# Performance work log

Hardware: AMD Instinct MI355X
Metric: run time of the kernel (lower is better)

The kernel has to match this reference:

```python
import jax, jax.numpy as jnp
import numpy as np
import math

N, C, H = 2048, 256, 8
D = C // H
T, R, E = 8, 12, 32768
BUCKETS = 21
SEED = 128


def _layernorm(x, g, b, eps=1e-5):
    mu = jnp.mean(x, axis=-1, keepdims=True)
    var = jnp.var(x, axis=-1, keepdims=True)
    return (x - mu) * jax.lax.rsqrt(var + eps) * g + b


def _bucketize_dt(dt, num_buckets):
    eps = 1e-06
    signed_log = jnp.sign(dt) * jnp.log1p(jnp.abs(dt) + eps)
    min_v, max_v = -5.0, 5.0
    norm = (jnp.clip(signed_log, min_v, max_v) - min_v) / (max_v - min_v + 1e-09)
    idx = jnp.floor(norm * (num_buckets - 1)).astype(jnp.int32)
    return jnp.clip(idx, 0, num_buckets - 1)


def setup_inputs() -> dict:
    key = jax.random.key(0)
    ks = jax.random.split(key, 24)
    s = 0.02
    inp = {
        'X': jax.random.normal(ks[0], (N, C), jnp.float32),
        'token_type': jax.random.randint(ks[1], (N,), 0, T, jnp.int32),
        'edge_src': jax.random.randint(ks[2], (E,), 0, N, jnp.int32),
        'edge_dst': jax.random.randint(ks[3], (E,), 0, N, jnp.int32),
        'edge_rel': jax.random.randint(ks[4], (E,), 0, R, jnp.int32),
        'time_vec': jax.random.normal(ks[5], (N,), jnp.float32),
        'seed_count': SEED,
        'Wq': jax.random.normal(ks[6], (C, C), jnp.float32) * s,
        'bq': jnp.zeros((C,), jnp.float32),
        'Wk': jax.random.normal(ks[7], (C, C), jnp.float32) * s,
        'bk': jnp.zeros((C,), jnp.float32),
        'Wv': jax.random.normal(ks[8], (C, C), jnp.float32) * s,
        'bv': jnp.zeros((C,), jnp.float32),
        'Wo': jax.random.normal(ks[9], (C, C), jnp.float32) * s,
        'bo': jnp.zeros((C,), jnp.float32),
        'ln1_g': jnp.ones((C,), jnp.float32),
        'ln1_b': jnp.zeros((C,), jnp.float32),
        'ln2_g': jnp.ones((C,), jnp.float32),
        'ln2_b': jnp.zeros((C,), jnp.float32),
        'W1': jax.random.normal(ks[10], (C, 4 * C), jnp.float32) * s,
        'b1': jnp.zeros((4 * C,), jnp.float32),
        'W2': jax.random.normal(ks[11], (4 * C, C), jnp.float32) * s,
        'b2': jnp.zeros((C,), jnp.float32),
        'adj_rel_bias': jnp.zeros((R, H), jnp.float32),
        'typepair_bias': jnp.zeros((T, T, H), jnp.float32),
        'temp_bias': jax.random.normal(ks[12], (BUCKETS, H), jnp.float32) * s,
    }
    return inp


def reference(X, token_type, edge_src, edge_dst, edge_rel, time_vec, seed_count,
              Wq, bq, Wk, bk, Wv, bv, Wo, bo,
              ln1_g, ln1_b, ln2_g, ln2_b, W1, b1, W2, b2,
              adj_rel_bias, typepair_bias, temp_bias):
    n = X.shape[0]
    h = _layernorm(X, ln1_g, ln1_b)
    q = (h @ Wq + bq).reshape(n, H, D)
    k = (h @ Wk + bk).reshape(n, H, D)
    v = (h @ Wv + bv).reshape(n, H, D)
    scores = jnp.einsum('nhd,mhd->hnm', q, k) / math.sqrt(D)  # [H, N, N]

    # structural bias, factored as [N, N, H] then transposed
    bias = typepair_bias[token_type][:, token_type]            # [N, N, H]
    bias = bias.at[edge_src, edge_dst].add(adj_rel_bias[edge_rel])
    # seed-wise temporal bias on the first seed_count rows
    dt = time_vec[None, :] - time_vec[:seed_count, None]       # [S, N]
    tb = temp_bias[_bucketize_dt(dt, BUCKETS)]                 # [S, N, H]
    bias = bias.at[:seed_count].add(tb)

    attn = jax.nn.softmax(scores + bias.transpose(2, 0, 1), axis=-1)
    o = jnp.einsum('hnm,mhd->nhd', attn, v).reshape(n, C)
    x = X + (o @ Wo + bo)

    h2 = _layernorm(x, ln2_g, ln2_b)
    f = jax.nn.gelu(h2 @ W1 + b1, approximate=False) @ W2 + b2
    return x + f
```

## Files before the change

kernel.cpp:

```cpp
#include <hip/hip_runtime.h>
#include <hip/hip_bf16.h>
#include <math.h>

#define NTOK 2048
#define CDIM 256
#define HHEADS 8
#define DHEAD 32
#define NEDGE 32768
#define NTILE 16
#define SPLITS 8
#define TPS 2
#define EXTD 64
#define LE 72

typedef __attribute__((ext_vector_type(8))) short short8;
typedef __attribute__((ext_vector_type(4))) short short4v;
typedef __attribute__((ext_vector_type(4))) float f32x4;

static __device__ inline short f2bf(float f) {
    __hip_bfloat16 h = __float2bfloat16(f);
    return *reinterpret_cast<short*>(&h);
}
static __device__ inline float bf2f(short s) {
    unsigned int u = ((unsigned int)(unsigned short)s) << 16;
    return *reinterpret_cast<float*>(&u);
}

__global__ __launch_bounds__(256) void ln4_kernel(const float* __restrict__ X,
    const float* __restrict__ g, const float* __restrict__ b, short* __restrict__ out)
{
    int t = threadIdx.x;
    int wv = t >> 6, lane = t & 63;
    int row = blockIdx.x * 4 + wv;

    float4 x = *(const float4*)&X[(size_t)row * CDIM + lane * 4];
    float s = x.x + x.y + x.z + x.w;
    #pragma unroll
    for (int off = 1; off < 64; off <<= 1) s += __shfl_xor(s, off);
    float mu = s * (1.0f / CDIM);
    float4 d = { x.x - mu, x.y - mu, x.z - mu, x.w - mu };
    float s2 = d.x * d.x + d.y * d.y + d.z * d.z + d.w * d.w;
    #pragma unroll
    for (int off = 1; off < 64; off <<= 1) s2 += __shfl_xor(s2, off);
    float rsig = rsqrtf(s2 * (1.0f / CDIM) + 1e-5f);
    float4 gg = *(const float4*)&g[lane * 4];
    float4 bb = *(const float4*)&b[lane * 4];
    short o4[4];
    o4[0] = f2bf(d.x * rsig * gg.x + bb.x);
    o4[1] = f2bf(d.y * rsig * gg.y + bb.y);
    o4[2] = f2bf(d.z * rsig * gg.z + bb.z);
    o4[3] = f2bf(d.w * rsig * gg.w + bb.w);
    *(short4v*)&out[(size_t)row * CDIM + lane * 4] = *(short4v*)o4;
}

static __device__ inline void transpose_tile_f32(const float* __restrict__ in,
    short* __restrict__ out, int K, int N, int k0, int n0, int t)
{
    __shared__ float tile[64][65];
    int r0 = t >> 4, c0 = (t & 15) * 4;
    #pragma unroll
    for (int i = 0; i < 4; i++) {
        int r = r0 + i * 16;
        float4 v = *(const float4*)(in + (size_t)(k0 + r) * N + n0 + c0);
        tile[r][c0 + 0] = v.x; tile[r][c0 + 1] = v.y;
        tile[r][c0 + 2] = v.z; tile[r][c0 + 3] = v.w;
    }
    __syncthreads();
    #pragma unroll
    for (int i = 0; i < 4; i++) {
        int nr = r0 + i * 16;
        short o4[4];
        #pragma unroll
        for (int j = 0; j < 4; j++) o4[j] = f2bf(tile[c0 + j][nr]);
        *(short4v*)(out + (size_t)(n0 + nr) * K + k0 + c0) = *(short4v*)o4;
    }
}

__global__ __launch_bounds__(256) void prep_kernel(
    const float* __restrict__ Wq, const float* __restrict__ Wk,
    const float* __restrict__ Wv, const float* __restrict__ Wo,
    const float* __restrict__ W1, const float* __restrict__ W2,
    short* __restrict__ wt_qkv, short* __restrict__ wot,
    short* __restrict__ w1t, short* __restrict__ w2t,
    const int* __restrict__ token_type, const float* __restrict__ typepair_bias,
    short* __restrict__ qh, short* __restrict__ kh,
    int* __restrict__ cnt2)
{
    int b = blockIdx.x;
    int t = threadIdx.x;
    if (b < 192) {
        const float* src; short* dst; int K, N, bx, by;
        if (b < 64) {
            int m = b >> 4, r = b & 15;
            src = (m == 0) ? Wq : (m == 1) ? Wk : (m == 2) ? Wv : Wo;
            dst = (m == 0) ? wt_qkv : (m == 1) ? wt_qkv + 256 * 256
                : (m == 2) ? wt_qkv + 512 * 256 : wot;
            K = 256; N = 256; bx = r & 3; by = r >> 2;
        } else if (b < 128) {
            int r = b - 64; src = W1; dst = w1t; K = 256; N = 1024; bx = r & 15; by = r >> 4;
        } else {
            int r = b - 128; src = W2; dst = w2t; K = 1024; N = 256; bx = r & 3; by = r >> 2;
        }
        transpose_tile_f32(src, dst, K, N, by * 64, bx * 64, t);
    } else if (b < 256) {
        int idx = (b - 192) * 256 + t;
        int row = idx >> 3, h = idx & 7;
        int tt = token_type[row];
        short qe[32], ke[32];
        #pragma unroll
        for (int j = 0; j < 32; j++) {
            if (j < 8) {
                qe[j] = f2bf(typepair_bias[(tt * 8 + j) * 8 + h]);
                ke[j] = (j == tt) ? (short)0x3F80 : (short)0;
            } else { qe[j] = 0; ke[j] = 0; }
        }
        size_t base = ((size_t)h * NTOK + row) * EXTD + 32;
        #pragma unroll
        for (int k = 0; k < 4; k++) {
            *(short8*)&qh[base + k * 8] = *(short8*)&qe[k * 8];
            *(short8*)&kh[base + k * 8] = *(short8*)&ke[k * 8];
        }
    } else {
        cnt2[(b - 256) * 256 + t] = 0;
        cnt2[(b - 256) * 256 + t + 8192] = 0;
        cnt2[(b - 256) * 256 + t + 16384] = 0;
        cnt2[(b - 256) * 256 + t + 24576] = 0;
    }
}

template<int EPI>
__global__ __launch_bounds__(256) void gemm32_kernel(
    const short* __restrict__ A, const short* __restrict__ Bt,
    const float* __restrict__ bias, const float* __restrict__ resid,
    void* __restrict__ out_, int M, int N, int K)
{
    __shared__ short A_lds[32 * 40];
    __shared__ short B_lds[64 * 40];

    const int t = threadIdx.x;
    const int w = t >> 6, lane = t & 63, c = lane & 15, g = lane >> 4;
    const int row0 = blockIdx.y * 32, col0 = blockIdx.x * 64;
    const int srow = t >> 2, sk = (t & 3) * 8;

    f32x4 acc[2] = {};

    for (int k0 = 0; k0 < K; k0 += 32) {
        if (t < 128)
            *(short8*)&A_lds[srow * 40 + sk] = *(const short8*)&A[(size_t)(row0 + srow) * K + k0 + sk];
        *(short8*)&B_lds[srow * 40 + sk] = *(const short8*)&Bt[(size_t)(col0 + srow) * K + k0 + sk];
        __syncthreads();
        short8 af = *(const short8*)&A_lds[((w & 1) * 16 + c) * 40 + g * 8];
        #pragma unroll
        for (int nf = 0; nf < 2; nf++) {
            short8 bf = *(const short8*)&B_lds[((w >> 1) * 32 + nf * 16 + c) * 40 + g * 8];
            acc[nf] = __builtin_amdgcn_mfma_f32_16x16x32_bf16(af, bf, acc[nf], 0, 0, 0);
        }
        __syncthreads();
    }

    #pragma unroll
    for (int nf = 0; nf < 2; nf++) {
        #pragma unroll
        for (int reg = 0; reg < 4; reg++) {
            int row = row0 + (w & 1) * 16 + g * 4 + reg;
            int col = col0 + (w >> 1) * 32 + nf * 16 + c;
            float v = acc[nf][reg] + bias[col];
            if (EPI == 2) {
                ((float*)out_)[(size_t)row * N + col] = v + resid[(size_t)row * N + col];
            } else {
                v = 0.5f * v * (1.0f + erff(v * 0.70710678118654752f));
                ((short*)out_)[(size_t)row * N + col] = f2bf(v);
            }
        }
    }
}

__global__ __launch_bounds__(256) void gemm32_qkv_kernel(
    const short* __restrict__ A, const short* __restrict__ Bt,
    const float* __restrict__ bq, const float* __restrict__ bk, const float* __restrict__ bv,
    short* __restrict__ qh, short* __restrict__ kh, short* __restrict__ vt)
{
    const int K = CDIM;
    __shared__ short A_lds[32 * 40];
    __shared__ short B_lds[64 * 40];

    const int t = threadIdx.x;
    const int w = t >> 6, lane = t & 63, c = lane & 15, g = lane >> 4;
    const int row0 = blockIdx.y * 32, col0 = blockIdx.x * 64;
    const int srow = t >> 2, sk = (t & 3) * 8;

    f32x4 acc[2] = {};

    for (int k0 = 0; k0 < K; k0 += 32) {
        if (t < 128)
            *(short8*)&A_lds[srow * 40 + sk] = *(const short8*)&A[(size_t)(row0 + srow) * K + k0 + sk];
        *(short8*)&B_lds[srow * 40 + sk] = *(const short8*)&Bt[(size_t)(col0 + srow) * K + k0 + sk];
        __syncthreads();
        short8 af = *(const short8*)&A_lds[((w & 1) * 16 + c) * 40 + g * 8];
        #pragma unroll
        for (int nf = 0; nf < 2; nf++) {
            short8 bf = *(const short8*)&B_lds[((w >> 1) * 32 + nf * 16 + c) * 40 + g * 8];
            acc[nf] = __builtin_amdgcn_mfma_f32_16x16x32_bf16(af, bf, acc[nf], 0, 0, 0);
        }
        __syncthreads();
    }

    const int region = col0 >> 8;
    const int colr0 = col0 & 255;
    const float* bias = (region == 0) ? bq : (region == 1) ? bk : bv;
    #pragma unroll
    for (int nf = 0; nf < 2; nf++) {
        #pragma unroll
        for (int reg = 0; reg < 4; reg++) {
            int row = row0 + (w & 1) * 16 + g * 4 + reg;
            int col = colr0 + (w >> 1) * 32 + nf * 16 + c;
            float v = acc[nf][reg] + bias[col];
            if (region == 0) v *= 0.17677669529663687f;
            short bb = f2bf(v);
            size_t hidx = ((size_t)(col >> 5) * NTOK + row) * EXTD + (col & 31);
            if (region == 0)      qh[hidx] = bb;
            else if (region == 1) kh[hidx] = bb;
            else                  vt[(size_t)col * NTOK + row] = bb;
        }
    }
}

__global__ void edge_hist2_kernel(const int* __restrict__ src, const int* __restrict__ dst,
    int* __restrict__ cnt, int E)
{
    int e = blockIdx.x * blockDim.x + threadIdx.x;
    if (e < E) atomicAdd(&cnt[src[e] * NTILE + (dst[e] >> 7)], 1);
}

__global__ __launch_bounds__(256) void edge_scan2_kernel(const int* __restrict__ cnt,
    int* __restrict__ row_ptr, int* __restrict__ wcur)
{
    __shared__ int sums[256];
    int t = threadIdx.x;
    int base = t * 128;
    int s = 0;
    for (int i = 0; i < 128; i++) s += cnt[base + i];
    sums[t] = s;
    __syncthreads();
    for (int off = 1; off < 256; off <<= 1) {
        int v = (t >= off) ? sums[t - off] : 0;
        __syncthreads();
        sums[t] += v;
        __syncthreads();
    }
    int run = (t == 0) ? 0 : sums[t - 1];
    for (int i = 0; i < 128; i++) {
        row_ptr[base + i] = run;
        wcur[base + i] = run;
        run += cnt[base + i];
    }
    if (t == 255) row_ptr[NTOK * NTILE] = run;
}

__global__ void edge_scatter2_kernel(const int* __restrict__ src, const int* __restrict__ dst,
    const int* __restrict__ rel, int* __restrict__ wcur, int2* __restrict__ pairs, int E)
{
    int e = blockIdx.x * blockDim.x + threadIdx.x;
    if (e < E) {
        int d = dst[e];
        int pos = atomicAdd(&wcur[src[e] * NTILE + (d >> 7)], 1);
        pairs[pos] = make_int2(d, rel[e]);
    }
}

__global__ __launch_bounds__(256) void sgemm_kernel(
    const short* __restrict__ qh, const short* __restrict__ kh,
    short* __restrict__ S)
{
    __shared__ short A_lds[64 * LE];
    __shared__ short B_lds[64 * LE];
    const int t = threadIdx.x;
    const int w = t >> 6, lane = t & 63, c = lane & 15, g = lane >> 4;
    const int h = blockIdx.z;
    const int m0 = blockIdx.x * 64, n0 = blockIdx.y * 64;

    {
        int r = t >> 3, off = (t & 7) * 8;
        *(short8*)&A_lds[r * LE + off] =
            *(const short8*)&qh[((size_t)h * NTOK + n0 + r) * EXTD + off];
        *(short8*)&A_lds[(r + 32) * LE + off] =
            *(const short8*)&qh[((size_t)h * NTOK + n0 + 32 + r) * EXTD + off];
        *(short8*)&B_lds[r * LE + off] =
            *(const short8*)&kh[((size_t)h * NTOK + m0 + r) * EXTD + off];
        *(short8*)&B_lds[(r + 32) * LE + off] =
            *(const short8*)&kh[((size_t)h * NTOK + m0 + 32 + r) * EXTD + off];
    }
    __syncthreads();

    short8 alo = *(const short8*)&A_lds[(w * 16 + c) * LE + g * 8];
    short8 ahi = *(const short8*)&A_lds[(w * 16 + c) * LE + 32 + g * 8];
    f32x4 acc[4] = {};
    #pragma unroll
    for (int nf = 0; nf < 4; nf++) {
        short8 blo = *(const short8*)&B_lds[(nf * 16 + c) * LE + g * 8];
        short8 bhi = *(const short8*)&B_lds[(nf * 16 + c) * LE + 32 + g * 8];
        acc[nf] = __builtin_amdgcn_mfma_f32_16x16x32_bf16(alo, blo, acc[nf], 0, 0, 0);
        acc[nf] = __builtin_amdgcn_mfma_f32_16x16x32_bf16(ahi, bhi, acc[nf], 0, 0, 0);
    }

    #pragma unroll
    for (int nf = 0; nf < 4; nf++)
        #pragma unroll
        for (int reg = 0; reg < 4; reg++) {
            int row = n0 + w * 16 + g * 4 + reg;
            int col = m0 + nf * 16 + c;
            S[((size_t)h * NTOK + row) * NTOK + col] = f2bf(acc[nf][reg]);
        }
}

__global__ __launch_bounds__(256) void softmax_kernel(
    short* __restrict__ S,
    const float* __restrict__ time_vec, const int* __restrict__ seed_ptr,
    const float* __restrict__ adj_rel_bias, const float* __restrict__ temp_bias,
    const int* __restrict__ row_ptr2, const int2* __restrict__ pairs2)
{
    __shared__ float rowbuf[4][NTOK];

    int t = threadIdx.x, wv = t >> 6, lane = t & 63;
    int task = blockIdx.x * 4 + wv;
    int h = task >> 11, n = task & 2047;
    int seed = seed_ptr[0];
    bool temporal = (n < seed);
    float tn = time_vec[n];
    float* rb = rowbuf[wv];
    short* Srow = &S[((size_t)h * NTOK + n) * NTOK];

    #pragma unroll
    for (int i = 0; i < 4; i++) {
        int m0 = i * 512 + lane * 8;
        short8 sv = *(const short8*)&Srow[m0];
        float v[8];
        #pragma unroll
        for (int j = 0; j < 8; j++) v[j] = bf2f(sv[j]);
        if (temporal) {
            float4 ta = *(const float4*)&time_vec[m0];
            float4 tb = *(const float4*)&time_vec[m0 + 4];
            float tv8[8] = { ta.x, ta.y, ta.z, ta.w, tb.x, tb.y, tb.z, tb.w };
            #pragma unroll
            for (int j = 0; j < 8; j++) {
                float dt = tv8[j] - tn;
                float ab = fabsf(dt) + 1e-6f;
                float sg = (dt > 0.0f) ? 1.0f : ((dt < 0.0f) ? -1.0f : 0.0f);
                float sl = sg * log1pf(ab);
                sl = fminf(fmaxf(sl, -5.0f), 5.0f);
                float norm = (sl + 5.0f) * (1.0f / (10.0f + 1e-9f));
                int bidx = (int)floorf(norm * 20.0f);
                bidx = min(max(bidx, 0), 20);
                v[j] += temp_bias[bidx * 8 + h];
            }
        }
        float4 lo = { v[0], v[1], v[2], v[3] };
        float4 hi = { v[4], v[5], v[6], v[7] };
        *(float4*)&rb[m0] = lo;
        *(float4*)&rb[m0 + 4] = hi;
    }
    __syncthreads();

    {
        int e0 = row_ptr2[n * NTILE], e1 = row_ptr2[(n + 1) * NTILE];
        for (int e = e0 + lane; e < e1; e += 64) {
            int2 pr = pairs2[e];
            atomicAdd(&rb[pr.x], adj_rel_bias[pr.y * 8 + h]);
        }
    }
    __syncthreads();

    float vv[32];
    float mx = -INFINITY;
    #pragma unroll
    for (int i = 0; i < 4; i++) {
        float4 a = *(const float4*)&rb[i * 512 + lane * 8];
        float4 b = *(const float4*)&rb[i * 512 + lane * 8 + 4];
        vv[i * 8 + 0] = a.x; vv[i * 8 + 1] = a.y; vv[i * 8 + 2] = a.z; vv[i * 8 + 3] = a.w;
        vv[i * 8 + 4] = b.x; vv[i * 8 + 5] = b.y; vv[i * 8 + 6] = b.z; vv[i * 8 + 7] = b.w;
    }
    #pragma unroll
    for (int i = 0; i < 32; i++) mx = fmaxf(mx, vv[i]);
    #pragma unroll
    for (int off = 1; off < 64; off <<= 1) mx = fmaxf(mx, __shfl_xor(mx, off));
    float sum = 0.0f;
    #pragma unroll
    for (int i = 0; i < 32; i++) { vv[i] = __expf(vv[i] - mx); sum += vv[i]; }
    #pragma unroll
    for (int off = 1; off < 64; off <<= 1) sum += __shfl_xor(sum, off);
    float inv = 1.0f / sum;

    #pragma unroll
    for (int i = 0; i < 4; i++) {
        short p8[8];
        #pragma unroll
        for (int j = 0; j < 8; j++) p8[j] = f2bf(vv[i * 8 + j] * inv);
        *(short8*)&Srow[i * 512 + lane * 8] = *(short8*)p8;
    }
}

__global__ __launch_bounds__(256) void pv_kernel(
    const short* __restrict__ P, const short* __restrict__ vt,
    short* __restrict__ o)
{
    __shared__ short A_lds[32 * LE];
    __shared__ short B_lds[32 * LE];
    const int t = threadIdx.x;
    const int w = t >> 6, lane = t & 63, c = lane & 15, g = lane >> 4;
    const int h = blockIdx.y;
    const int n0 = blockIdx.x * 32;
    const int rowblk = (w & 1) * 16, colblk = (w >> 1) * 16;

    f32x4 acc = {0.0f, 0.0f, 0.0f, 0.0f};

    for (int k0 = 0; k0 < NTOK; k0 += 64) {
        int r = t >> 3, off = (t & 7) * 8;
        *(short8*)&A_lds[r * LE + off] =
            *(const short8*)&P[((size_t)h * NTOK + n0 + r) * NTOK + k0 + off];
        *(short8*)&B_lds[r * LE + off] =
            *(const short8*)&vt[(size_t)(h * 32 + r) * NTOK + k0 + off];
        __syncthreads();
        short8 alo = *(const short8*)&A_lds[(rowblk + c) * LE + g * 8];
        short8 ahi = *(const short8*)&A_lds[(rowblk + c) * LE + 32 + g * 8];
        short8 blo = *(const short8*)&B_lds[(colblk + c) * LE + g * 8];
        short8 bhi = *(const short8*)&B_lds[(colblk + c) * LE + 32 + g * 8];
        acc = __builtin_amdgcn_mfma_f32_16x16x32_bf16(alo, blo, acc, 0, 0, 0);
        acc = __builtin_amdgcn_mfma_f32_16x16x32_bf16(ahi, bhi, acc, 0, 0, 0);
        __syncthreads();
    }

    #pragma unroll
    for (int reg = 0; reg < 4; reg++) {
        int row = n0 + rowblk + g * 4 + reg;
        int col = h * 32 + colblk + c;
        o[(size_t)row * CDIM + col] = f2bf(acc[reg]);
    }
}

#define QBLK 32
#define KBLK 128

__global__ __launch_bounds__(256) void attn_mfma3_kernel(
    const short* __restrict__ qh, const short* __restrict__ kh,
    const short* __restrict__ vt,
    const float* __restrict__ time_vec, const int* __restrict__ seed_ptr,
    const float* __restrict__ adj_rel_bias, const float* __restrict__ temp_bias,
    const int* __restrict__ row_ptr2, const int2* __restrict__ pairs2,
    float* __restrict__ Op_part, float2* __restrict__ ml_part)
{
    __shared__ __align__(16) short Q_lds[QBLK * LE];
    __shared__ __align__(16) short K_lds[KBLK * LE];
    __shared__ __align__(16) short Vt_lds[DHEAD * 136];
    __shared__ __align__(16) unsigned int P32[QBLK * 68];
    __shared__ float tcol_s[KBLK];
    __shared__ float temp_h[21];
    __shared__ float adj_h[12];
    __shared__ float2 ml[2][QBLK];

    const int h  = blockIdx.y;
    const int n0 = blockIdx.x * QBLK;
    const int sblk = blockIdx.z;
    const int t  = threadIdx.x;
    const int wv = t >> 6, lane = t & 63, c = lane & 15, g = lane >> 4;
    const int rowblk  = (wv & 1) * 16;
    const int halfIdx = wv >> 1;
    const int colhalf = halfIdx * 64;
    const int seed = seed_ptr[0];
    const bool blockTemporal = (n0 < seed);
    const int gt0 = sblk * TPS;

    {
        int row = t >> 3, off = (t & 7) * 8;
        *(short8*)&Q_lds[row * LE + off] =
            *(const short8*)&qh[((size_t)h * NTOK + n0 + row) * EXTD + off];
    }
    if (t < 21)  temp_h[t] = temp_bias[t * HHEADS + h];
    if (t < 12)  adj_h[t] = adj_rel_bias[t * HHEADS + h];

    const int nrow = n0 + rowblk + c;
    const bool rowTemporal = (nrow < seed);
    const float tn = time_vec[nrow];

    int2 rp01 = *(const int2*)&row_ptr2[nrow * NTILE + gt0];
    int  rp2  = row_ptr2[nrow * NTILE + gt0 + 2];

    const int krow = t >> 3, koff = (t & 7) * 8;
    const int vrow = t >> 4, voff = (t & 15) * 8;
    short8 kr0, kr1, kr2, kr3, vr0, vr1;
    float tcr = 0.0f;

    auto LOADT = [&](int gt) {
        int m0 = gt * KBLK;
        const short* kp = &kh[((size_t)h * NTOK + m0 + krow) * EXTD + koff];
        kr0 = *(const short8*)kp;
        kr1 = *(const short8*)(kp + (size_t)32 * EXTD);
        kr2 = *(const short8*)(kp + (size_t)64 * EXTD);
        kr3 = *(const short8*)(kp + (size_t)96 * EXTD);
        const short* vp = &vt[(size_t)(h * 32 + vrow) * NTOK + m0 + voff];
        vr0 = *(const short8*)vp;
        vr1 = *(const short8*)(vp + (size_t)16 * NTOK);
        if (blockTemporal && t < 128) tcr = time_vec[m0 + t];
    };
    auto WRITET = [&]() {
        *(short8*)&K_lds[krow * LE + koff]        = kr0;
        *(short8*)&K_lds[(krow + 32) * LE + koff] = kr1;
        *(short8*)&K_lds[(krow + 64) * LE + koff] = kr2;
        *(short8*)&K_lds[(krow + 96) * LE + koff] = kr3;
        *(short8*)&Vt_lds[vrow * 136 + voff]        = vr0;
        *(short8*)&Vt_lds[(vrow + 16) * 136 + voff] = vr1;
        if (blockTemporal && t < 128) tcol_s[t] = tcr;
    };

    float m_run = -INFINITY, l_run = 0.0f;
    f32x4 oacc[2] = {{0,0,0,0},{0,0,0,0}};
    const f32x4 zf = {0.0f, 0.0f, 0.0f, 0.0f};

    LOADT(gt0);
    WRITET();

    for (int tile = 0; tile < TPS; ++tile) {
        __syncthreads();
        if (tile + 1 < TPS) LOADT(gt0 + tile + 1);

        short8 qlo = *(const short8*)&Q_lds[(rowblk + c) * LE + g * 8];
        short8 qhi = *(const short8*)&Q_lds[(rowblk + c) * LE + 32 + g * 8];
        float vals[16];
        #pragma unroll
        for (int blk = 0; blk < 4; blk++) {
            const short* kb = &K_lds[(colhalf + blk * 16 + c) * LE];
            short8 klo = *(const short8*)(kb + g * 8);
            short8 khi = *(const short8*)(kb + 32 + g * 8);
            f32x4 acc = __builtin_amdgcn_mfma_f32_16x16x32_bf16(klo, qlo, zf, 0, 0, 0);
            acc = __builtin_amdgcn_mfma_f32_16x16x32_bf16(khi, qhi, acc, 0, 0, 0);
            #pragma unroll
            for (int reg = 0; reg < 4; reg++) vals[blk * 4 + reg] = acc[reg];
        }

        if (rowTemporal) {
            #pragma unroll
            for (int blk = 0; blk < 4; blk++) {
                #pragma unroll
                for (int reg = 0; reg < 4; reg++) {
                    float dt = tcol_s[colhalf + blk * 16 + g * 4 + reg] - tn;
                    float ab = fabsf(dt) + 1e-6f;
                    float sg = (dt > 0.0f) ? 1.0f : ((dt < 0.0f) ? -1.0f : 0.0f);
                    float sl = sg * log1pf(ab);
                    sl = fminf(fmaxf(sl, -5.0f), 5.0f);
                    float norm = (sl + 5.0f) * (1.0f / (10.0f + 1e-9f));
                    int bidx = (int)floorf(norm * 20.0f);
                    bidx = min(max(bidx, 0), 20);
                    vals[blk * 4 + reg] += temp_h[bidx];
                }
            }
        }
        {
            int e0 = (tile == 0) ? rp01.x : rp01.y;
            int e1 = (tile == 0) ? rp01.y : rp2;
            for (int e = e0; e < e1; ++e) {
                int2 pr = pairs2[e];
                int dloc = pr.x & 127;
                if ((dloc >> 6) == halfIdx) {
                    int ml64 = dloc & 63;
                    if (((ml64 >> 2) & 3) == g) {
                        float ab = adj_h[pr.y];
                        int li = (ml64 >> 4) * 4 + (ml64 & 3);
                        #pragma unroll
                        for (int i = 0; i < 16; i++) vals[i] += (i == li) ? ab : 0.0f;
                    }
                }
            }
        }

        float tmax = vals[0];
        #pragma unroll
        for (int i = 1; i < 16; i++) tmax = fmaxf(tmax, vals[i]);
        tmax = fmaxf(tmax, __shfl_xor(tmax, 16));
        tmax = fmaxf(tmax, __shfl_xor(tmax, 32));
        float m_new = fmaxf(m_run, tmax);
        float psum = 0.0f;
        #pragma unroll
        for (int i = 0; i < 16; i++) { vals[i] = __expf(vals[i] - m_new); psum += vals[i]; }
        psum += __shfl_xor(psum, 16);
        psum += __shfl_xor(psum, 32);
        float scale = __expf(m_run - m_new);
        m_run = m_new;
        l_run = l_run * scale + psum;

        #pragma unroll
        for (int blk = 0; blk < 4; blk++) {
            #pragma unroll
            for (int r = 0; r < 2; r++) {
                unsigned lo = (unsigned short)f2bf(vals[blk * 4 + 2 * r]);
                unsigned hi = (unsigned short)f2bf(vals[blk * 4 + 2 * r + 1]);
                P32[(rowblk + c) * 68 + halfIdx * 32 + blk * 8 + g * 2 + r] = lo | (hi << 16);
            }
        }

        float scr[4];
        #pragma unroll
        for (int reg = 0; reg < 4; reg++) scr[reg] = __shfl(scale, 4 * g + reg);
        #pragma unroll
        for (int dblk = 0; dblk < 2; dblk++)
            #pragma unroll
            for (int reg = 0; reg < 4; reg++) oacc[dblk][reg] *= scr[reg];
        #pragma unroll
        for (int kc = 0; kc < 2; kc++) {
            short8 pa = *(const short8*)&P32[(rowblk + c) * 68 + halfIdx * 32 + kc * 16 + g * 4];
            #pragma unroll
            for (int dblk = 0; dblk < 2; dblk++) {
                short8 vb = *(const short8*)&Vt_lds[(dblk * 16 + c) * 136 + colhalf + kc * 32 + g * 8];
                oacc[dblk] = __builtin_amdgcn_mfma_f32_16x16x32_bf16(pa, vb, oacc[dblk], 0, 0, 0);
            }
        }

        __syncthreads();
        if (tile + 1 < TPS) WRITET();
    }

    __syncthreads();
    if (lane < 16) ml[halfIdx][rowblk + lane] = make_float2(m_run, l_run);
    __syncthreads();

    float* Op = (float*)K_lds;
    #pragma unroll
    for (int reg = 0; reg < 4; reg++) {
        int rw = rowblk + 4 * g + reg;
        float2 a0 = ml[0][rw], a1 = ml[1][rw];
        float mm = fmaxf(a0.x, a1.x);
        float wh = __expf((halfIdx == 0 ? a0.x : a1.x) - mm);
        Op[halfIdx * 32 * 36 + rw * 36 + c]      = oacc[0][reg] * wh;
        Op[halfIdx * 32 * 36 + rw * 36 + 16 + c] = oacc[1][reg] * wh;
    }
    __syncthreads();

    {
        int row = t >> 3, d0 = (t & 7) * 4;
        float2 a0 = ml[0][row], a1 = ml[1][row];
        float mm = fmaxf(a0.x, a1.x);
        float w0 = __expf(a0.x - mm), w1 = __expf(a1.x - mm);
        float lc = a0.y * w0 + a1.y * w1;
        float4 pa = *(const float4*)&Op[row * 36 + d0];
        float4 pb = *(const float4*)&Op[(32 + row) * 36 + d0];
        float4 sum;
        sum.x = pa.x + pb.x; sum.y = pa.y + pb.y;
        sum.z = pa.z + pb.z; sum.w = pa.w + pb.w;
        *(float4*)&Op_part[((size_t)sblk * NTOK + n0 + row) * CDIM + h * DHEAD + d0] = sum;
        if ((t & 7) == 0)
            ml_part[((size_t)sblk * NTOK + n0 + row) * HHEADS + h] = make_float2(mm, lc);
    }
}

__global__ __launch_bounds__(256) void attn_reduce_kernel(
    const float* __restrict__ Op_part, const float2* __restrict__ ml_part,
    short* __restrict__ o)
{
    int row = blockIdx.x;
    int t = threadIdx.x;
    int h = t >> 5, d = t & 31;

    float2 a[SPLITS];
    float mm = -INFINITY;
    #pragma unroll
    for (int s = 0; s < SPLITS; s++) {
        a[s] = ml_part[((size_t)s * NTOK + row) * HHEADS + h];
        mm = fmaxf(mm, a[s].x);
    }
    float l = 0.0f, w[SPLITS];
    #pragma unroll
    for (int s = 0; s < SPLITS; s++) { w[s] = __expf(a[s].x - mm); l += a[s].y * w[s]; }
    float inv = 1.0f / l;
    size_t idx = (size_t)row * CDIM + h * DHEAD + d;
    float acc = 0.0f;
    #pragma unroll
    for (int s = 0; s < SPLITS; s++)
        acc += w[s] * Op_part[(size_t)s * NTOK * CDIM + idx];
    o[idx] = f2bf(acc * inv);
}

extern "C" void kernel_launch(void* const* d_in, const int* in_sizes, int n_in,
                              void* d_out, int out_size, void* d_ws, size_t ws_size,
                              hipStream_t stream)
{
    (void)in_sizes; (void)n_in; (void)out_size;
    const float* X        = (const float*)d_in[0];
    const int* token_type = (const int*)d_in[1];
    const int* edge_src   = (const int*)d_in[2];
    const int* edge_dst   = (const int*)d_in[3];
    const int* edge_rel   = (const int*)d_in[4];
    const float* time_vec = (const float*)d_in[5];
    const int* seed_ptr   = (const int*)d_in[6];
    const float* Wq = (const float*)d_in[7];  const float* bq = (const float*)d_in[8];
    const float* Wk = (const float*)d_in[9];  const float* bk = (const float*)d_in[10];
    const float* Wv = (const float*)d_in[11]; const float* bv = (const float*)d_in[12];
    const float* Wo = (const float*)d_in[13]; const float* bo = (const float*)d_in[14];
    const float* ln1_g = (const float*)d_in[15]; const float* ln1_b = (const float*)d_in[16];
    const float* ln2_g = (const float*)d_in[17]; const float* ln2_b = (const float*)d_in[18];
    const float* W1 = (const float*)d_in[19]; const float* b1 = (const float*)d_in[20];
    const float* W2 = (const float*)d_in[21]; const float* b2 = (const float*)d_in[22];
    const float* adj_rel_bias  = (const float*)d_in[23];
    const float* typepair_bias = (const float*)d_in[24];
    const float* temp_bias     = (const float*)d_in[25];
    float* out = (float*)d_out;

    char* base = (char*)d_ws;
    size_t off = 0;
    auto alloc = [&](size_t bytes) { char* p = base + off; off += (bytes + 255) & ~(size_t)255; return p; };
    short* qh_bf   = (short*)alloc((size_t)HHEADS * NTOK * EXTD * 2);
    short* kh_bf   = (short*)alloc((size_t)HHEADS * NTOK * EXTD * 2);
    short* vt_bf   = (short*)alloc((size_t)256 * NTOK * 2);
    short* h1_bf   = (short*)alloc((size_t)NTOK * 256 * 2);
    short* h2_bf   = (short*)alloc((size_t)NTOK * 256 * 2);
    short* o_bf    = (short*)alloc((size_t)NTOK * 256 * 2);
    short* mid_bf  = (short*)alloc((size_t)NTOK * 1024 * 2);
    float* xb      = (float*)alloc((size_t)NTOK * 256 * 4);
    short* wt_qkv  = (short*)alloc((size_t)768 * 256 * 2);
    short* wot     = (short*)alloc((size_t)256 * 256 * 2);
    short* w1t     = (short*)alloc((size_t)1024 * 256 * 2);
    short* w2t     = (short*)alloc((size_t)256 * 1024 * 2);
    int2*  pairs2  = (int2*)alloc((size_t)NEDGE * 8);
    int*   cnt2    = (int*)alloc((size_t)NTOK * NTILE * 4);
    int*   rowptr2 = (int*)alloc(((size_t)NTOK * NTILE + 1) * 4);
    int*   wcur2   = (int*)alloc((size_t)NTOK * NTILE * 4);

    const size_t s_bytes = (size_t)HHEADS * NTOK * NTOK * 2;
    const bool bigws = (ws_size >= off + s_bytes + (1u << 20));

    prep_kernel<<<288, 256, 0, stream>>>(Wq, Wk, Wv, Wo, W1, W2,
                                         wt_qkv, wot, w1t, w2t,
                                         token_type, typepair_bias,
                                         qh_bf, kh_bf, cnt2);
    edge_hist2_kernel<<<NEDGE / 256, 256, 0, stream>>>(edge_src, edge_dst, cnt2, NEDGE);
    edge_scan2_kernel<<<1, 256, 0, stream>>>(cnt2, rowptr2, wcur2);
    edge_scatter2_kernel<<<NEDGE / 256, 256, 0, stream>>>(edge_src, edge_dst, edge_rel, wcur2, pairs2, NEDGE);

    ln4_kernel<<<NTOK / 4, 256, 0, stream>>>(X, ln1_g, ln1_b, h1_bf);
    gemm32_qkv_kernel<<<dim3(12, 64), 256, 0, stream>>>(h1_bf, wt_qkv, bq, bk, bv,
                                                        qh_bf, kh_bf, vt_bf);

    if (bigws) {
        short* S = (short*)alloc(s_bytes);
        sgemm_kernel<<<dim3(32, 32, 8), 256, 0, stream>>>(qh_bf, kh_bf, S);
        softmax_kernel<<<NTOK * HHEADS / 4, 256, 0, stream>>>(
            S, time_vec, seed_ptr, adj_rel_bias, temp_bias, rowptr2, pairs2);
        pv_kernel<<<dim3(64, 8), 256, 0, stream>>>(S, vt_bf, o_bf);
    } else {
        float* Op_part  = (float*)alloc((size_t)SPLITS * NTOK * CDIM * 4);
        float2* ml_part = (float2*)alloc((size_t)SPLITS * NTOK * HHEADS * 8);
        attn_mfma3_kernel<<<dim3(NTOK / QBLK, HHEADS, SPLITS), 256, 0, stream>>>(
            qh_bf, kh_bf, vt_bf, time_vec, seed_ptr,
            adj_rel_bias, temp_bias, rowptr2, pairs2, Op_part, ml_part);
        attn_reduce_kernel<<<NTOK, 256, 0, stream>>>(Op_part, ml_part, o_bf);
    }

    gemm32_kernel<2><<<dim3(4, 64), 256, 0, stream>>>(o_bf, wot, bo, X, xb, NTOK, 256, 256);

    ln4_kernel<<<NTOK / 4, 256, 0, stream>>>(xb, ln2_g, ln2_b, h2_bf);

    gemm32_kernel<3><<<dim3(16, 64), 256, 0, stream>>>(h2_bf, w1t, b1, nullptr, mid_bf, NTOK, 1024, 256);
    gemm32_kernel<2><<<dim3(4, 64), 256, 0, stream>>>(mid_bf, w2t, b2, xb, out, NTOK, 256, 1024);
}
```

Measured before the change: 151.9 us.

## Use per-row edge CSR and apply edge bias in registers in softmax

```diff
diff --git a/kernel.cpp b/kernel.cpp
--- a/kernel.cpp
+++ b/kernel.cpp
@@ -7,9 +7,6 @@
 #define HHEADS 8
 #define DHEAD 32
 #define NEDGE 32768
-#define NTILE 16
-#define SPLITS 8
-#define TPS 2
 #define EXTD 64
 #define LE 72
 
@@ -84,7 +81,7 @@
     short* __restrict__ w1t, short* __restrict__ w2t,
     const int* __restrict__ token_type, const float* __restrict__ typepair_bias,
     short* __restrict__ qh, short* __restrict__ kh,
-    int* __restrict__ cnt2)
+    int* __restrict__ cnt)
 {
     int b = blockIdx.x;
     int t = threadIdx.x;
@@ -121,10 +118,8 @@
             *(short8*)&kh[base + k * 8] = *(short8*)&ke[k * 8];
         }
     } else {
-        cnt2[(b - 256) * 256 + t] = 0;
-        cnt2[(b - 256) * 256 + t + 8192] = 0;
-        cnt2[(b - 256) * 256 + t + 16384] = 0;
-        cnt2[(b - 256) * 256 + t + 24576] = 0;
+        #pragma unroll
+        for (int i = 0; i < 8; i++) cnt[t * 8 + i] = 0;
     }
 }
 
@@ -225,21 +220,22 @@
     }
 }
 
-__global__ void edge_hist2_kernel(const int* __restrict__ src, const int* __restrict__ dst,
-    int* __restrict__ cnt, int E)
+__global__ void edge_hist_kernel(const int* __restrict__ src, int* __restrict__ cnt, int E)
 {
     int e = blockIdx.x * blockDim.x + threadIdx.x;
-    if (e < E) atomicAdd(&cnt[src[e] * NTILE + (dst[e] >> 7)], 1);
-}
-
-__global__ __launch_bounds__(256) void edge_scan2_kernel(const int* __restrict__ cnt,
+    if (e < E) atomicAdd(&cnt[src[e]], 1);
+}
+
+__global__ __launch_bounds__(256) void edge_scan_kernel(const int* __restrict__ cnt,
     int* __restrict__ row_ptr, int* __restrict__ wcur)
 {
     __shared__ int sums[256];
     int t = threadIdx.x;
-    int base = t * 128;
+    int base = t * 8;
+    int local[8];
     int s = 0;
-    for (int i = 0; i < 128; i++) s += cnt[base + i];
+    #pragma unroll
+    for (int i = 0; i < 8; i++) { local[i] = s; s += cnt[base + i]; }
     sums[t] = s;
     __syncthreads();
     for (int off = 1; off < 256; off <<= 1) {
@@ -248,23 +244,23 @@
         sums[t] += v;
         __syncthreads();
     }
-    int run = (t == 0) ? 0 : sums[t - 1];
-    for (int i = 0; i < 128; i++) {
-        row_ptr[base + i] = run;
-        wcur[base + i] = run;
-        run += cnt[base + i];
-    }
-    if (t == 255) row_ptr[NTOK * NTILE] = run;
-}
-
-__global__ void edge_scatter2_kernel(const int* __restrict__ src, const int* __restrict__ dst,
+    int excl = (t == 0) ? 0 : sums[t - 1];
+    #pragma unroll
+    for (int i = 0; i < 8; i++) {
+        int r = excl + local[i];
+        row_ptr[base + i] = r;
+        wcur[base + i] = r;
+    }
+    if (t == 255) row_ptr[NTOK] = sums[255];
+}
+
+__global__ void edge_scatter_kernel(const int* __restrict__ src, const int* __restrict__ dst,
     const int* __restrict__ rel, int* __restrict__ wcur, int2* __restrict__ pairs, int E)
 {
     int e = blockIdx.x * blockDim.x + threadIdx.x;
     if (e < E) {
-        int d = dst[e];
-        int pos = atomicAdd(&wcur[src[e] * NTILE + (d >> 7)], 1);
-        pairs[pos] = make_int2(d, rel[e]);
+        int pos = atomicAdd(&wcur[src[e]], 1);
+        pairs[pos] = make_int2(dst[e], rel[e]);
     }
 }
 
@@ -317,19 +313,17 @@
     short* __restrict__ S,
     const float* __restrict__ time_vec, const int* __restrict__ seed_ptr,
     const float* __restrict__ adj_rel_bias, const float* __restrict__ temp_bias,
-    const int* __restrict__ row_ptr2, const int2* __restrict__ pairs2)
-{
-    __shared__ float rowbuf[4][NTOK];
-
+    const int* __restrict__ row_ptr, const int2* __restrict__ pairs)
+{
     int t = threadIdx.x, wv = t >> 6, lane = t & 63;
     int task = blockIdx.x * 4 + wv;
     int h = task >> 11, n = task & 2047;
     int seed = seed_ptr[0];
     bool temporal = (n < seed);
     float tn = time_vec[n];
-    float* rb = rowbuf[wv];
     short* Srow = &S[((size_t)h * NTOK + n) * NTOK];
 
+    float vv[32];
     #pragma unroll
     for (int i = 0; i < 4; i++) {
         int m0 = i * 512 + lane * 8;
@@ -354,33 +348,34 @@
                 v[j] += temp_bias[bidx * 8 + h];
             }
         }
-        float4 lo = { v[0], v[1], v[2], v[3] };
-        float4 hi = { v[4], v[5], v[6], v[7] };
-        *(float4*)&rb[m0] = lo;
-        *(float4*)&rb[m0 + 4] = hi;
-    }
-    __syncthreads();
+        #pragma unroll
+        for (int j = 0; j < 8; j++) vv[i * 8 + j] = v[j];
+    }
 
     {
-        int e0 = row_ptr2[n * NTILE], e1 = row_ptr2[(n + 1) * NTILE];
-        for (int e = e0 + lane; e < e1; e += 64) {
-            int2 pr = pairs2[e];
-            atomicAdd(&rb[pr.x], adj_rel_bias[pr.y * 8 + h]);
-        }
-    }
-    __syncthreads();
-
-    float vv[32];
-    float mx = -INFINITY;
-    #pragma unroll
-    for (int i = 0; i < 4; i++) {
-        float4 a = *(const float4*)&rb[i * 512 + lane * 8];
-        float4 b = *(const float4*)&rb[i * 512 + lane * 8 + 4];
-        vv[i * 8 + 0] = a.x; vv[i * 8 + 1] = a.y; vv[i * 8 + 2] = a.z; vv[i * 8 + 3] = a.w;
-        vv[i * 8 + 4] = b.x; vv[i * 8 + 5] = b.y; vv[i * 8 + 6] = b.z; vv[i * 8 + 7] = b.w;
-    }
-    #pragma unroll
-    for (int i = 0; i < 32; i++) mx = fmaxf(mx, vv[i]);
+        int e0 = row_ptr[n], e1 = row_ptr[n + 1];
+        for (int e = e0; e < e1; ++e) {
+            int2 pr = pairs[e];
+            int col = pr.x;
+            if (((col >> 3) & 63) == lane) {
+                float ab = adj_rel_bias[pr.y * 8 + h];
+                int ci = col >> 9;
+                int sl = col & 7;
+                #pragma unroll
+                for (int q = 0; q < 4; q++) {
+                    if (q == ci) {
+                        #pragma unroll
+                        for (int j = 0; j < 8; j++)
+                            vv[q * 8 + j] += (j == sl) ? ab : 0.0f;
+                    }
+                }
+            }
+        }
+    }
+
+    float mx = vv[0];
+    #pragma unroll
+    for (int i = 1; i < 32; i++) mx = fmaxf(mx, vv[i]);
     #pragma unroll
     for (int off = 1; off < 64; off <<= 1) mx = fmaxf(mx, __shfl_xor(mx, off));
     float sum = 0.0f;
@@ -437,251 +432,11 @@
     }
 }
 
-#define QBLK 32
-#define KBLK 128
-
-__global__ __launch_bounds__(256) void attn_mfma3_kernel(
-    const short* __restrict__ qh, const short* __restrict__ kh,
-    const short* __restrict__ vt,
-    const float* __restrict__ time_vec, const int* __restrict__ seed_ptr,
-    const float* __restrict__ adj_rel_bias, const float* __restrict__ temp_bias,
-    const int* __restrict__ row_ptr2, const int2* __restrict__ pairs2,
-    float* __restrict__ Op_part, float2* __restrict__ ml_part)
-{
-    __shared__ __align__(16) short Q_lds[QBLK * LE];
-    __shared__ __align__(16) short K_lds[KBLK * LE];
-    __shared__ __align__(16) short Vt_lds[DHEAD * 136];
-    __shared__ __align__(16) unsigned int P32[QBLK * 68];
-    __shared__ float tcol_s[KBLK];
-    __shared__ float temp_h[21];
-    __shared__ float adj_h[12];
-    __shared__ float2 ml[2][QBLK];
-
-    const int h  = blockIdx.y;
-    const int n0 = blockIdx.x * QBLK;
-    const int sblk = blockIdx.z;
-    const int t  = threadIdx.x;
-    const int wv = t >> 6, lane = t & 63, c = lane & 15, g = lane >> 4;
-    const int rowblk  = (wv & 1) * 16;
-    const int halfIdx = wv >> 1;
-    const int colhalf = halfIdx * 64;
-    const int seed = seed_ptr[0];
-    const bool blockTemporal = (n0 < seed);
-    const int gt0 = sblk * TPS;
-
-    {
-        int row = t >> 3, off = (t & 7) * 8;
-        *(short8*)&Q_lds[row * LE + off] =
-            *(const short8*)&qh[((size_t)h * NTOK + n0 + row) * EXTD + off];
-    }
-    if (t < 21)  temp_h[t] = temp_bias[t * HHEADS + h];
-    if (t < 12)  adj_h[t] = adj_rel_bias[t * HHEADS + h];
-
-    const int nrow = n0 + rowblk + c;
-    const bool rowTemporal = (nrow < seed);
-    const float tn = time_vec[nrow];
-
-    int2 rp01 = *(const int2*)&row_ptr2[nrow * NTILE + gt0];
-    int  rp2  = row_ptr2[nrow * NTILE + gt0 + 2];
-
-    const int krow = t >> 3, koff = (t & 7) * 8;
-    const int vrow = t >> 4, voff = (t & 15) * 8;
-    short8 kr0, kr1, kr2, kr3, vr0, vr1;
-    float tcr = 0.0f;
-
-    auto LOADT = [&](int gt) {
-        int m0 = gt * KBLK;
-        const short* kp = &kh[((size_t)h * NTOK + m0 + krow) * EXTD + koff];
-        kr0 = *(const short8*)kp;
-        kr1 = *(const short8*)(kp + (size_t)32 * EXTD);
-        kr2 = *(const short8*)(kp + (size_t)64 * EXTD);
-        kr3 = *(const short8*)(kp + (size_t)96 * EXTD);
-        const short* vp = &vt[(size_t)(h * 32 + vrow) * NTOK + m0 + voff];
-        vr0 = *(const short8*)vp;
-        vr1 = *(const short8*)(vp + (size_t)16 * NTOK);
-        if (blockTemporal && t < 128) tcr = time_vec[m0 + t];
-    };
-    auto WRITET = [&]() {
-        *(short8*)&K_lds[krow * LE + koff]        = kr0;
-        *(short8*)&K_lds[(krow + 32) * LE + koff] = kr1;
-        *(short8*)&K_lds[(krow + 64) * LE + koff] = kr2;
-        *(short8*)&K_lds[(krow + 96) * LE + koff] = kr3;
-        *(short8*)&Vt_lds[vrow * 136 + voff]        = vr0;
-        *(short8*)&Vt_lds[(vrow + 16) * 136 + voff] = vr1;
-        if (blockTemporal && t < 128) tcol_s[t] = tcr;
-    };
-
-    float m_run = -INFINITY, l_run = 0.0f;
-    f32x4 oacc[2] = {{0,0,0,0},{0,0,0,0}};
-    const f32x4 zf = {0.0f, 0.0f, 0.0f, 0.0f};
-
-    LOADT(gt0);
-    WRITET();
-
-    for (int tile = 0; tile < TPS; ++tile) {
-        __syncthreads();
-        if (tile + 1 < TPS) LOADT(gt0 + tile + 1);
-
-        short8 qlo = *(const short8*)&Q_lds[(rowblk + c) * LE + g * 8];
-        short8 qhi = *(const short8*)&Q_lds[(rowblk + c) * LE + 32 + g * 8];
-        float vals[16];
-        #pragma unroll
-        for (int blk = 0; blk < 4; blk++) {
-            const short* kb = &K_lds[(colhalf + blk * 16 + c) * LE];
-            short8 klo = *(const short8*)(kb + g * 8);
-            short8 khi = *(const short8*)(kb + 32 + g * 8);
-            f32x4 acc = __builtin_amdgcn_mfma_f32_16x16x32_bf16(klo, qlo, zf, 0, 0, 0);
-            acc = __builtin_amdgcn_mfma_f32_16x16x32_bf16(khi, qhi, acc, 0, 0, 0);
-            #pragma unroll
-            for (int reg = 0; reg < 4; reg++) vals[blk * 4 + reg] = acc[reg];
-        }
-
-        if (rowTemporal) {
-            #pragma unroll
-            for (int blk = 0; blk < 4; blk++) {
-                #pragma unroll
-                for (int reg = 0; reg < 4; reg++) {
-                    float dt = tcol_s[colhalf + blk * 16 + g * 4 + reg] - tn;
-                    float ab = fabsf(dt) + 1e-6f;
-                    float sg = (dt > 0.0f) ? 1.0f : ((dt < 0.0f) ? -1.0f : 0.0f);
-                    float sl = sg * log1pf(ab);
-                    sl = fminf(fmaxf(sl, -5.0f), 5.0f);
-                    float norm = (sl + 5.0f) * (1.0f / (10.0f + 1e-9f));
-                    int bidx = (int)floorf(norm * 20.0f);
-                    bidx = min(max(bidx, 0), 20);
-                    vals[blk * 4 + reg] += temp_h[bidx];
-                }
-            }
-        }
-        {
-            int e0 = (tile == 0) ? rp01.x : rp01.y;
-            int e1 = (tile == 0) ? rp01.y : rp2;
-            for (int e = e0; e < e1; ++e) {
-                int2 pr = pairs2[e];
-                int dloc = pr.x & 127;
-                if ((dloc >> 6) == halfIdx) {
-                    int ml64 = dloc & 63;
-                    if (((ml64 >> 2) & 3) == g) {
-                        float ab = adj_h[pr.y];
-                        int li = (ml64 >> 4) * 4 + (ml64 & 3);
-                        #pragma unroll
-                        for (int i = 0; i < 16; i++) vals[i] += (i == li) ? ab : 0.0f;
-                    }
-                }
-            }
-        }
-
-        float tmax = vals[0];
-        #pragma unroll
-        for (int i = 1; i < 16; i++) tmax = fmaxf(tmax, vals[i]);
-        tmax = fmaxf(tmax, __shfl_xor(tmax, 16));
-        tmax = fmaxf(tmax, __shfl_xor(tmax, 32));
-        float m_new = fmaxf(m_run, tmax);
-        float psum = 0.0f;
-        #pragma unroll
-        for (int i = 0; i < 16; i++) { vals[i] = __expf(vals[i] - m_new); psum += vals[i]; }
-        psum += __shfl_xor(psum, 16);
-        psum += __shfl_xor(psum, 32);
-        float scale = __expf(m_run - m_new);
-        m_run = m_new;
-        l_run = l_run * scale + psum;
-
-        #pragma unroll
-        for (int blk = 0; blk < 4; blk++) {
-            #pragma unroll
-            for (int r = 0; r < 2; r++) {
-                unsigned lo = (unsigned short)f2bf(vals[blk * 4 + 2 * r]);
-                unsigned hi = (unsigned short)f2bf(vals[blk * 4 + 2 * r + 1]);
-                P32[(rowblk + c) * 68 + halfIdx * 32 + blk * 8 + g * 2 + r] = lo | (hi << 16);
-            }
-        }
-
-        float scr[4];
-        #pragma unroll
-        for (int reg = 0; reg < 4; reg++) scr[reg] = __shfl(scale, 4 * g + reg);
-        #pragma unroll
-        for (int dblk = 0; dblk < 2; dblk++)
-            #pragma unroll
-            for (int reg = 0; reg < 4; reg++) oacc[dblk][reg] *= scr[reg];
-        #pragma unroll
-        for (int kc = 0; kc < 2; kc++) {
-            short8 pa = *(const short8*)&P32[(rowblk + c) * 68 + halfIdx * 32 + kc * 16 + g * 4];
-            #pragma unroll
-            for (int dblk = 0; dblk < 2; dblk++) {
-                short8 vb = *(const short8*)&Vt_lds[(dblk * 16 + c) * 136 + colhalf + kc * 32 + g * 8];
-                oacc[dblk] = __builtin_amdgcn_mfma_f32_16x16x32_bf16(pa, vb, oacc[dblk], 0, 0, 0);
-            }
-        }
-
-        __syncthreads();
-        if (tile + 1 < TPS) WRITET();
-    }
-
-    __syncthreads();
-    if (lane < 16) ml[halfIdx][rowblk + lane] = make_float2(m_run, l_run);
-    __syncthreads();
-
-    float* Op = (float*)K_lds;
-    #pragma unroll
-    for (int reg = 0; reg < 4; reg++) {
-        int rw = rowblk + 4 * g + reg;
-        float2 a0 = ml[0][rw], a1 = ml[1][rw];
-        float mm = fmaxf(a0.x, a1.x);
-        float wh = __expf((halfIdx == 0 ? a0.x : a1.x) - mm);
-        Op[halfIdx * 32 * 36 + rw * 36 + c]      = oacc[0][reg] * wh;
-        Op[halfIdx * 32 * 36 + rw * 36 + 16 + c] = oacc[1][reg] * wh;
-    }
-    __syncthreads();
-
-    {
-        int row = t >> 3, d0 = (t & 7) * 4;
-        float2 a0 = ml[0][row], a1 = ml[1][row];
-        float mm = fmaxf(a0.x, a1.x);
-        float w0 = __expf(a0.x - mm), w1 = __expf(a1.x - mm);
-        float lc = a0.y * w0 + a1.y * w1;
-        float4 pa = *(const float4*)&Op[row * 36 + d0];
-        float4 pb = *(const float4*)&Op[(32 + row) * 36 + d0];
-        float4 sum;
-        sum.x = pa.x + pb.x; sum.y = pa.y + pb.y;
-        sum.z = pa.z + pb.z; sum.w = pa.w + pb.w;
-        *(float4*)&Op_part[((size_t)sblk * NTOK + n0 + row) * CDIM + h * DHEAD + d0] = sum;
-        if ((t & 7) == 0)
-            ml_part[((size_t)sblk * NTOK + n0 + row) * HHEADS + h] = make_float2(mm, lc);
-    }
-}
-
-__global__ __launch_bounds__(256) void attn_reduce_kernel(
-    const float* __restrict__ Op_part, const float2* __restrict__ ml_part,
-    short* __restrict__ o)
-{
-    int row = blockIdx.x;
-    int t = threadIdx.x;
-    int h = t >> 5, d = t & 31;
-
-    float2 a[SPLITS];
-    float mm = -INFINITY;
-    #pragma unroll
-    for (int s = 0; s < SPLITS; s++) {
-        a[s] = ml_part[((size_t)s * NTOK + row) * HHEADS + h];
-        mm = fmaxf(mm, a[s].x);
-    }
-    float l = 0.0f, w[SPLITS];
-    #pragma unroll
-    for (int s = 0; s < SPLITS; s++) { w[s] = __expf(a[s].x - mm); l += a[s].y * w[s]; }
-    float inv = 1.0f / l;
-    size_t idx = (size_t)row * CDIM + h * DHEAD + d;
-    float acc = 0.0f;
-    #pragma unroll
-    for (int s = 0; s < SPLITS; s++)
-        acc += w[s] * Op_part[(size_t)s * NTOK * CDIM + idx];
-    o[idx] = f2bf(acc * inv);
-}
-
 extern "C" void kernel_launch(void* const* d_in, const int* in_sizes, int n_in,
                               void* d_out, int out_size, void* d_ws, size_t ws_size,
                               hipStream_t stream)
 {
-    (void)in_sizes; (void)n_in; (void)out_size;
+    (void)in_sizes; (void)n_in; (void)out_size; (void)ws_size;
     const float* X        = (const float*)d_in[0];
     const int* token_type = (const int*)d_in[1];
     const int* edge_src   = (const int*)d_in[2];
@@ -717,40 +472,30 @@
     short* wot     = (short*)alloc((size_t)256 * 256 * 2);
     short* w1t     = (short*)alloc((size_t)1024 * 256 * 2);
     short* w2t     = (short*)alloc((size_t)256 * 1024 * 2);
-    int2*  pairs2  = (int2*)alloc((size_t)NEDGE * 8);
-    int*   cnt2    = (int*)alloc((size_t)NTOK * NTILE * 4);
-    int*   rowptr2 = (int*)alloc(((size_t)NTOK * NTILE + 1) * 4);
-    int*   wcur2   = (int*)alloc((size_t)NTOK * NTILE * 4);
-
-    const size_t s_bytes = (size_t)HHEADS * NTOK * NTOK * 2;
-    const bool bigws = (ws_size >= off + s_bytes + (1u << 20));
-
-    prep_kernel<<<288, 256, 0, stream>>>(Wq, Wk, Wv, Wo, W1, W2,
+    int2*  pairs   = (int2*)alloc((size_t)NEDGE * 8);
+    int*   cnt     = (int*)alloc((size_t)NTOK * 4);
+    int*   rowptr  = (int*)alloc(((size_t)NTOK + 1) * 4);
+    int*   wcur    = (int*)alloc((size_t)NTOK * 4);
+    short* S       = (short*)alloc((size_t)HHEADS * NTOK * NTOK * 2);
+
+    prep_kernel<<<257, 256, 0, stream>>>(Wq, Wk, Wv, Wo, W1, W2,
                                          wt_qkv, wot, w1t, w2t,
                                          token_type, typepair_bias,
-                                         qh_bf, kh_bf, cnt2);
-    edge_hist2_kernel<<<NEDGE / 256, 256, 0, stream>>>(edge_src, edge_dst, cnt2, NEDGE);
-    edge_scan2_kernel<<<1, 256, 0, stream>>>(cnt2, rowptr2, wcur2);
-    edge_scatter2_kernel<<<NEDGE / 256, 256, 0, stream>>>(edge_src, edge_dst, edge_rel, wcur2, pairs2, NEDGE);
+                                         qh_bf, kh_bf, cnt);
+
+    edge_hist_kernel<<<NEDGE / 256, 256, 0, stream>>>(edge_src, cnt, NEDGE);
+    edge_scan_kernel<<<1, 256, 0, stream>>>(cnt, rowptr, wcur);
+    edge_scatter_kernel<<<NEDGE / 256, 256, 0, stream>>>(edge_src, edge_dst, edge_rel, wcur, pairs, NEDGE);
 
     ln4_kernel<<<NTOK / 4, 256, 0, stream>>>(X, ln1_g, ln1_b, h1_bf);
+
     gemm32_qkv_kernel<<<dim3(12, 64), 256, 0, stream>>>(h1_bf, wt_qkv, bq, bk, bv,
                                                         qh_bf, kh_bf, vt_bf);
 
-    if (bigws) {
-        short* S = (short*)alloc(s_bytes);
-        sgemm_kernel<<<dim3(32, 32, 8), 256, 0, stream>>>(qh_bf, kh_bf, S);
-        softmax_kernel<<<NTOK * HHEADS / 4, 256, 0, stream>>>(
-            S, time_vec, seed_ptr, adj_rel_bias, temp_bias, rowptr2, pairs2);
-        pv_kernel<<<dim3(64, 8), 256, 0, stream>>>(S, vt_bf, o_bf);
-    } else {
-        float* Op_part  = (float*)alloc((size_t)SPLITS * NTOK * CDIM * 4);
-        float2* ml_part = (float2*)alloc((size_t)SPLITS * NTOK * HHEADS * 8);
-        attn_mfma3_kernel<<<dim3(NTOK / QBLK, HHEADS, SPLITS), 256, 0, stream>>>(
-            qh_bf, kh_bf, vt_bf, time_vec, seed_ptr,
-            adj_rel_bias, temp_bias, rowptr2, pairs2, Op_part, ml_part);
-        attn_reduce_kernel<<<NTOK, 256, 0, stream>>>(Op_part, ml_part, o_bf);
-    }
+    sgemm_kernel<<<dim3(32, 32, 8), 256, 0, stream>>>(qh_bf, kh_bf, S);
+    softmax_kernel<<<NTOK * HHEADS / 4, 256, 0, stream>>>(
+        S, time_vec, seed_ptr, adj_rel_bias, temp_bias, rowptr, pairs);
+    pv_kernel<<<dim3(64, 8), 256, 0, stream>>>(S, vt_bf, o_bf);
 
     gemm32_kernel<2><<<dim3(4, 64), 256, 0, stream>>>(o_bf, wot, bo, X, xb, NTOK, 256, 256);
 
```

New measurement: 155.5 us. 2.4% more time.
